# Optimization experiments

Hardware: AMD Instinct MI355X
Metric: run time of the kernel (lower is better)

Reference implementation:

```python
import jax, jax.numpy as jnp
import numpy as np
from jax import lax

# Module hyperparameters (init_kwargs)
FH, FW = 5, 5          # kernel_size
DIL_Y, DIL_X = 2, 2    # kernel_dilation
G = 2                  # num_deform_groups
F = 64                 # filters
K = FH * FW            # kernel taps


def setup_inputs() -> dict:
    key = jax.random.key(0)
    ks = jax.random.split(key, 4)
    B, H, W, C = 4, 128, 128, 32
    volume = jax.random.normal(ks[0], (B, H, W, C), jnp.float32)
    # offset-predicting conv params: offset_num = FH*FW*G*2 = 100 channels
    w_off = jax.random.normal(ks[1], (FH, FW, C, K * 2 * G), jnp.float32) * 0.01
    b_off = jnp.zeros((K * 2 * G,), jnp.float32)
    # deformable conv weights: (taps, in_channels, filters)
    w_dcn = jax.random.normal(ks[2], (K, C, F), jnp.float32) * (1.0 / np.sqrt(K * C))
    b_dcn = jnp.zeros((F,), jnp.float32)
    return {"volume": volume, "w_off": w_off, "b_off": b_off,
            "w_dcn": w_dcn, "b_dcn": b_dcn}


def _deform_conv(volume, w_off, b_off, w_dcn, b_dcn):
    B, H, W, C = volume.shape
    dp_y = DIL_Y * (FH // 2)  # dilated_pad_y
    dp_x = DIL_X * (FW // 2)  # dilated_pad_x

    # 1) dense offset conv (VALID, dilated) -> (B, oh, ow, K*2*G)
    offsets = lax.conv_general_dilated(
        volume, w_off, window_strides=(1, 1), padding='VALID',
        rhs_dilation=(DIL_Y, DIL_X),
        dimension_numbers=('NHWC', 'HWIO', 'NHWC')) + b_off
    oh, ow = offsets.shape[1], offsets.shape[2]
    off = offsets.reshape(B, oh, ow, K, 2, G)  # [..., (dy,dx), group]

    # 2) base sampling grid (stride 1): output pixel centers + dilated taps
    base_y = jnp.arange(dp_y, H - dp_y, dtype=volume.dtype)   # (oh,)
    base_x = jnp.arange(dp_x, W - dp_x, dtype=volume.dtype)   # (ow,)
    kys = jnp.arange(-dp_y, dp_y + 1, DIL_Y, dtype=volume.dtype)
    kxs = jnp.arange(-dp_x, dp_x + 1, DIL_X, dtype=volume.dtype)
    kus, kvs = jnp.meshgrid(kxs, kys)         # (FH, FW) as in source
    kdy = kvs.reshape(-1)                     # (K,)
    kdx = kus.reshape(-1)                     # (K,)

    # sample positions: (B, oh, ow, K, G)
    py = base_y[None, :, None, None, None] + kdy[None, None, None, :, None] + off[..., 0, :]
    px = base_x[None, None, :, None, None] + kdx[None, None, None, :, None] + off[..., 1, :]
    py = jnp.clip(py, 0.0, H - 1.0)
    px = jnp.clip(px, 0.0, W - 1.0)

    # 3) bilinear gather
    y0 = jnp.clip(jnp.floor(py), 0.0, H - 2.0)
    x0 = jnp.clip(jnp.floor(px), 0.0, W - 2.0)
    wy = (py - y0)[..., None]
    wx = (px - x0)[..., None]
    y0i = y0.astype(jnp.int32)
    x0i = x0.astype(jnp.int32)
    bidx = jnp.arange(B)[:, None, None, None, None]

    def gather(yy, xx):
        return volume[bidx, yy, xx]  # (B, oh, ow, K, G, C)

    v00 = gather(y0i, x0i)
    v01 = gather(y0i, x0i + 1)
    v10 = gather(y0i + 1, x0i)
    v11 = gather(y0i + 1, x0i + 1)
    sampled = (v00 * (1 - wy) * (1 - wx) + v01 * (1 - wy) * wx
               + v10 * wy * (1 - wx) + v11 * wy * wx)  # (B, oh, ow, K, G, C)

    # 4) weighted conv; deform groups partition the output filters
    wr = w_dcn.reshape(K, C, G, F // G)
    out = jnp.einsum('bhwkgc,kcgf->bhwgf', sampled, wr).reshape(B, oh, ow, F)
    return out + b_dcn


def reference(volume, w_off, b_off, w_dcn, b_dcn):
    return _deform_conv(volume, w_off, b_off, w_dcn, b_dcn)
```

## Files before the change

### kernel.cpp

```cpp
#include <hip/hip_runtime.h>
#include <hip/hip_fp16.h>

#define BB 4
#define HH 128
#define WW 128
#define CC 32
#define OH 120
#define OW 120
#define KT 25
#define OFFC 100
#define FF 64
#define NPX 32
#define NTHREADS 512

typedef __attribute__((ext_vector_type(8))) short    s16x8;
typedef __attribute__((ext_vector_type(8))) _Float16 f16x8;
typedef __attribute__((ext_vector_type(2))) _Float16 h2;
typedef __attribute__((ext_vector_type(4))) float    f32x4;

#define WB_ELEMS   (KT * 7 * 64 * 8)
#define WD_ELEMS   (4 * KT * 64 * 8)
#define VOL_UNITS  (BB * HH * WW * CC / 8)
#define VOL16_OFF  (WB_ELEMS + WD_ELEMS)

__device__ __forceinline__ short f2h(float x) {
    _Float16 h = (_Float16)x;
    return __builtin_bit_cast(short, h);
}
__device__ __forceinline__ float h2f(short x) {
    return (float)__builtin_bit_cast(_Float16, x);
}

__global__ __launch_bounds__(256) void repack_kernel(
    const float* __restrict__ volume, const float* __restrict__ w_off,
    const float* __restrict__ w_dcn, short* __restrict__ ws)
{
    int idx = blockIdx.x * 256 + threadIdx.x;
    short* WB  = ws;
    short* WD  = ws + WB_ELEMS;
    short* V16 = ws + VOL16_OFF;
    if (idx < WB_ELEMS) {
        int j = idx & 7, l = (idx >> 3) & 63;
        int tn = idx >> 9;
        int n = tn % 7, t = tn / 7;
        int c = (l >> 4) * 8 + j;
        int oc = n * 16 + (l & 15);
        float v = (oc < OFFC) ? w_off[(t * CC + c) * OFFC + oc] : 0.f;
        WB[idx] = f2h(v);
    } else if (idx < WB_ELEMS + WD_ELEMS) {
        int idx2 = idx - WB_ELEMS;
        int j = idx2 & 7, l = (idx2 >> 3) & 63;
        int nt = idx2 >> 9;
        int t = nt % KT, n = nt / KT;
        int c = (l >> 4) * 8 + j;
        int f = n * 16 + (l & 15);
        WD[idx2] = f2h(w_dcn[(t * CC + c) * FF + f]);
    } else {
        int v = idx - (WB_ELEMS + WD_ELEMS);
        if (v < VOL_UNITS) {
            const float* src = volume + (size_t)v * 8;
            float4 q0 = *(const float4*)src;
            float4 q1 = *(const float4*)(src + 4);
            alignas(16) short tmp[8];
            tmp[0] = f2h(q0.x); tmp[1] = f2h(q0.y); tmp[2] = f2h(q0.z); tmp[3] = f2h(q0.w);
            tmp[4] = f2h(q1.x); tmp[5] = f2h(q1.y); tmp[6] = f2h(q1.z); tmp[7] = f2h(q1.w);
            *(s16x8*)&V16[(size_t)v * 8] = *(const s16x8*)tmp;
        }
    }
}

__global__ __launch_bounds__(512, 2) void dcn_fused(
    const short* __restrict__ ws_ro, const float* __restrict__ b_off,
    const float* __restrict__ b_dcn, float* __restrict__ out)
{
    __shared__ __align__(16) char smem[59648];
    short* samp    = (short*)smem;
    short* patch   = (short*)smem;
    short* offtile = (short*)(smem + 53248);

    const short* WB  = ws_ro;
    const short* WD  = ws_ro + WB_ELEMS;
    const short* V16 = ws_ro + VOL16_OFF;

    const int tid  = threadIdx.x;
    const int lane = tid & 63;
    const int wv   = tid >> 6;
    const int ox0  = blockIdx.x * NPX;
    const int oy   = blockIdx.y;
    const int b    = blockIdx.z;
    const short* Vb = V16 + (size_t)b * (HH * WW * CC);

    for (int i = tid; i < 9 * 40 * 4; i += NTHREADS) {
        int cq = i & 3;
        int xi = (i >> 2) % 40;
        int yi = (i >> 2) / 40;
        int col = ox0 + xi; col = (col < WW) ? col : (WW - 1);
        s16x8 v = *(const s16x8*)&Vb[((size_t)(oy + yi) * WW + col) * CC + cq * 8];
        int u = ((yi * 40 + xi) << 2) + (cq ^ (xi & 3) ^ ((xi >> 2) & 3));
        *(s16x8*)&patch[u * 8] = v;
    }
    __syncthreads();

    if (wv < 7) {
        const int pr = lane & 15, cq = lane >> 4;
        f32x4 a0 = (f32x4){0.f, 0.f, 0.f, 0.f};
        f32x4 a1 = (f32x4){0.f, 0.f, 0.f, 0.f};
        for (int fh = 0; fh < 5; ++fh) {
            #pragma unroll
            for (int fw = 0; fw < 5; ++fw) {
                int t = fh * 5 + fw;
                int x0 = pr + 2 * fw, x1 = x0 + 16;
                f16x8 af0 = *(const f16x8*)&patch[((((2 * fh) * 40 + x0) << 2) + (cq ^ (x0 & 3) ^ ((x0 >> 2) & 3))) * 8];
                f16x8 af1 = *(const f16x8*)&patch[((((2 * fh) * 40 + x1) << 2) + (cq ^ (x1 & 3) ^ ((x1 >> 2) & 3))) * 8];
                f16x8 bf = *(const f16x8*)&WB[(t * 7 + wv) * 512 + lane * 8];
                a0 = __builtin_amdgcn_mfma_f32_16x16x32_f16(af0, bf, a0, 0, 0, 0);
                a1 = __builtin_amdgcn_mfma_f32_16x16x32_f16(af1, bf, a1, 0, 0, 0);
            }
        }
        int col = lane & 15, q = lane >> 4;
        int oc = wv * 16 + col;
        if (oc < OFFC) {
            float bo = b_off[oc];
            #pragma unroll
            for (int r = 0; r < 4; ++r) {
                offtile[(q * 4 + r) * 100 + oc]        = f2h(a0[r] + bo);
                offtile[(16 + q * 4 + r) * 100 + oc]   = f2h(a1[r] + bo);
            }
        }
    }
    __syncthreads();

    const int mt = wv & 1;
    const int ft = wv >> 1;
    const int g_ = ft >> 1;
    const int p_ = mt * 16 + (lane & 15);
    const int cq_ = lane >> 4;
    f32x4 acc = (f32x4){0.f, 0.f, 0.f, 0.f};

    for (int h = 0; h < 2; ++h) {
        const int tbase = h ? 13 : 0;
        const int ntap  = h ? 12 : 13;

        for (int u = tid; u < ntap * 256; u += NTHREADS) {
            int c  = u & 3;
            int p  = (u >> 2) & 31;
            int gg = (u >> 7) & 1;
            int tp = u >> 8;
            int t  = tbase + tp;
            int pe = (ox0 + p < OW) ? p : (OW - 1 - ox0);
            int t5 = t / 5, tm5 = t - t5 * 5;
            float dy = h2f(offtile[pe * 100 + t * 4 + gg]);
            float dx = h2f(offtile[pe * 100 + t * 4 + 2 + gg]);
            float py = (float)(oy + 2 * t5) + dy;
            float px = (float)(ox0 + pe + 2 * tm5) + dx;
            py = fminf(fmaxf(py, 0.f), 127.f);
            px = fminf(fmaxf(px, 0.f), 127.f);
            float y0f = fminf(floorf(py), 126.f);
            float x0f = fminf(floorf(px), 126.f);
            float wy = py - y0f, wx = px - x0f;
            int y0 = (int)y0f, x0i = (int)x0f;
            float w00 = (1.f - wy) * (1.f - wx);
            float w01 = (1.f - wy) * wx;
            float w10 = wy * (1.f - wx);
            float w11 = wy * wx;
            h2 W00 = (h2){(_Float16)w00, (_Float16)w00};
            h2 W01 = (h2){(_Float16)w01, (_Float16)w01};
            h2 W10 = (h2){(_Float16)w10, (_Float16)w10};
            h2 W11 = (h2){(_Float16)w11, (_Float16)w11};

            const short* vb0 = Vb + ((size_t)(y0 * WW + x0i)) * CC + c * 8;
            uint4 Au = *(const uint4*)(vb0);
            uint4 Bu = *(const uint4*)(vb0 + CC);
            uint4 Cu = *(const uint4*)(vb0 + WW * CC);
            uint4 Du = *(const uint4*)(vb0 + WW * CC + CC);

            uint4 res;
            {
                h2 r0 = __builtin_bit_cast(h2, Au.x) * W00;
                r0 = __builtin_elementwise_fma(__builtin_bit_cast(h2, Bu.x), W01, r0);
                r0 = __builtin_elementwise_fma(__builtin_bit_cast(h2, Cu.x), W10, r0);
                r0 = __builtin_elementwise_fma(__builtin_bit_cast(h2, Du.x), W11, r0);
                res.x = __builtin_bit_cast(unsigned, r0);
                h2 r1 = __builtin_bit_cast(h2, Au.y) * W00;
                r1 = __builtin_elementwise_fma(__builtin_bit_cast(h2, Bu.y), W01, r1);
                r1 = __builtin_elementwise_fma(__builtin_bit_cast(h2, Cu.y), W10, r1);
                r1 = __builtin_elementwise_fma(__builtin_bit_cast(h2, Du.y), W11, r1);
                res.y = __builtin_bit_cast(unsigned, r1);
                h2 r2 = __builtin_bit_cast(h2, Au.z) * W00;
                r2 = __builtin_elementwise_fma(__builtin_bit_cast(h2, Bu.z), W01, r2);
                r2 = __builtin_elementwise_fma(__builtin_bit_cast(h2, Cu.z), W10, r2);
                r2 = __builtin_elementwise_fma(__builtin_bit_cast(h2, Du.z), W11, r2);
                res.z = __builtin_bit_cast(unsigned, r2);
                h2 r3 = __builtin_bit_cast(h2, Au.w) * W00;
                r3 = __builtin_elementwise_fma(__builtin_bit_cast(h2, Bu.w), W01, r3);
                r3 = __builtin_elementwise_fma(__builtin_bit_cast(h2, Cu.w), W10, r3);
                r3 = __builtin_elementwise_fma(__builtin_bit_cast(h2, Du.w), W11, r3);
                res.w = __builtin_bit_cast(unsigned, r3);
            }
            int unit = (tp * 32 + p) * 8 + ((gg * 4 + c) ^ (p & 7));
            *(uint4*)&samp[unit * 8] = res;
        }
        __syncthreads();

        {
            const short* wd = WD + (ft * KT + tbase) * 512 + lane * 8;
            for (int tp = 0; tp < ntap; ++tp) {
                int unit = (tp * 32 + p_) * 8 + ((g_ * 4 + cq_) ^ (p_ & 7));
                f16x8 af = *(const f16x8*)&samp[unit * 8];
                f16x8 bf = *(const f16x8*)&wd[tp * 512];
                acc = __builtin_amdgcn_mfma_f32_16x16x32_f16(af, bf, acc, 0, 0, 0);
            }
        }
        __syncthreads();
    }

    {
        int col = lane & 15, q = lane >> 4;
        int f = ft * 16 + col;
        float bd = b_dcn[f];
        long pix0 = ((long)b * OH + oy) * OW + ox0;
        #pragma unroll
        for (int r = 0; r < 4; ++r) {
            int pp = mt * 16 + q * 4 + r;
            if (ox0 + pp < OW)
                out[(pix0 + pp) * FF + f] = acc[r] + bd;
        }
    }
}

extern "C" void kernel_launch(void* const* d_in, const int* in_sizes, int n_in,
                              void* d_out, int out_size, void* d_ws, size_t ws_size,
                              hipStream_t stream) {
    const float* volume = (const float*)d_in[0];
    const float* w_off  = (const float*)d_in[1];
    const float* b_off  = (const float*)d_in[2];
    const float* w_dcn  = (const float*)d_in[3];
    const float* b_dcn  = (const float*)d_in[4];
    float* out = (float*)d_out;
    short* ws  = (short*)d_ws;

    int repack_threads = WB_ELEMS + WD_ELEMS + VOL_UNITS;
    int repack_blocks  = (repack_threads + 255) / 256;
    repack_kernel<<<repack_blocks, 256, 0, stream>>>(volume, w_off, w_dcn, ws);

    dim3 g2((OW + NPX - 1) / NPX, OH, BB);
    dcn_fused<<<g2, NTHREADS, 0, stream>>>(ws, b_off, b_dcn, out);
}
```

Measured before the change: 127.1 us.

## Sample bilinear taps from an LDS halo window and fuse sampling into MFMA loop

Drops the fp16 copy of the whole volume made by the repack kernel. Each block now converts a 13x45 fp32 halo window straight into LDS. Bilinear taps that land inside the window are read from LDS; the rest fall back to global fp32 loads. Sample positions and weights are computed once into LDS, and each wave interpolates and feeds its result straight into two MFMAs. Tap halves are split across waves and reduced through LDS, with launch bounds raised to 4, at the cost of divergent fallback paths and higher register pressure.

Result: slower. 132.1 us (+4.0%).

```diff
diff --git a/kernel.cpp b/kernel.cpp
--- a/kernel.cpp
+++ b/kernel.cpp
@@ -13,6 +13,10 @@
 #define NPX 32
 #define NTHREADS 512
 
+#define WROWS 13
+#define WCOLS 45
+#define WUNITS (WROWS * WCOLS * 4)
+
 typedef __attribute__((ext_vector_type(8))) short    s16x8;
 typedef __attribute__((ext_vector_type(8))) _Float16 f16x8;
 typedef __attribute__((ext_vector_type(2))) _Float16 h2;
@@ -20,8 +24,6 @@
 
 #define WB_ELEMS   (KT * 7 * 64 * 8)
 #define WD_ELEMS   (4 * KT * 64 * 8)
-#define VOL_UNITS  (BB * HH * WW * CC / 8)
-#define VOL16_OFF  (WB_ELEMS + WD_ELEMS)
 
 __device__ __forceinline__ short f2h(float x) {
     _Float16 h = (_Float16)x;
@@ -30,15 +32,17 @@
 __device__ __forceinline__ float h2f(short x) {
     return (float)__builtin_bit_cast(_Float16, x);
 }
+__device__ __forceinline__ unsigned pk2(float a, float b) {
+    return ((unsigned)(unsigned short)f2h(a)) | (((unsigned)(unsigned short)f2h(b)) << 16);
+}
 
 __global__ __launch_bounds__(256) void repack_kernel(
-    const float* __restrict__ volume, const float* __restrict__ w_off,
-    const float* __restrict__ w_dcn, short* __restrict__ ws)
+    const float* __restrict__ w_off, const float* __restrict__ w_dcn,
+    short* __restrict__ ws)
 {
     int idx = blockIdx.x * 256 + threadIdx.x;
-    short* WB  = ws;
-    short* WD  = ws + WB_ELEMS;
-    short* V16 = ws + VOL16_OFF;
+    short* WB = ws;
+    short* WD = ws + WB_ELEMS;
     if (idx < WB_ELEMS) {
         int j = idx & 7, l = (idx >> 3) & 63;
         int tn = idx >> 9;
@@ -55,32 +59,26 @@
         int c = (l >> 4) * 8 + j;
         int f = n * 16 + (l & 15);
         WD[idx2] = f2h(w_dcn[(t * CC + c) * FF + f]);
-    } else {
-        int v = idx - (WB_ELEMS + WD_ELEMS);
-        if (v < VOL_UNITS) {
-            const float* src = volume + (size_t)v * 8;
-            float4 q0 = *(const float4*)src;
-            float4 q1 = *(const float4*)(src + 4);
-            alignas(16) short tmp[8];
-            tmp[0] = f2h(q0.x); tmp[1] = f2h(q0.y); tmp[2] = f2h(q0.z); tmp[3] = f2h(q0.w);
-            tmp[4] = f2h(q1.x); tmp[5] = f2h(q1.y); tmp[6] = f2h(q1.z); tmp[7] = f2h(q1.w);
-            *(s16x8*)&V16[(size_t)v * 8] = *(const s16x8*)tmp;
-        }
-    }
-}
-
-__global__ __launch_bounds__(512, 2) void dcn_fused(
-    const short* __restrict__ ws_ro, const float* __restrict__ b_off,
-    const float* __restrict__ b_dcn, float* __restrict__ out)
+    }
+}
+
+__device__ __forceinline__ int wunit(int q, int c) {
+    return q * 4 + (c ^ (q & 3));
+}
+
+__global__ __launch_bounds__(512, 4) void dcn_fused(
+    const float* __restrict__ volume, const short* __restrict__ ws_ro,
+    const float* __restrict__ b_off, const float* __restrict__ b_dcn,
+    float* __restrict__ out)
 {
-    __shared__ __align__(16) char smem[59648];
-    short* samp    = (short*)smem;
-    short* patch   = (short*)smem;
-    short* offtile = (short*)(smem + 53248);
-
-    const short* WB  = ws_ro;
-    const short* WD  = ws_ro + WB_ELEMS;
-    const short* V16 = ws_ro + VOL16_OFF;
+    __shared__ __align__(16) char smem[56640];
+    short*    window  = (short*)smem;
+    unsigned* pos4    = (unsigned*)(smem + 37440);
+    short*    offtile = (short*)(smem + 50240);
+    f32x4*    red     = (f32x4*)smem;
+
+    const short* WB = ws_ro;
+    const short* WD = ws_ro + WB_ELEMS;
 
     const int tid  = threadIdx.x;
     const int lane = tid & 63;
@@ -88,16 +86,22 @@
     const int ox0  = blockIdx.x * NPX;
     const int oy   = blockIdx.y;
     const int b    = blockIdx.z;
-    const short* Vb = V16 + (size_t)b * (HH * WW * CC);
-
-    for (int i = tid; i < 9 * 40 * 4; i += NTHREADS) {
-        int cq = i & 3;
-        int xi = (i >> 2) % 40;
-        int yi = (i >> 2) / 40;
-        int col = ox0 + xi; col = (col < WW) ? col : (WW - 1);
-        s16x8 v = *(const s16x8*)&Vb[((size_t)(oy + yi) * WW + col) * CC + cq * 8];
-        int u = ((yi * 40 + xi) << 2) + (cq ^ (xi & 3) ^ ((xi >> 2) & 3));
-        *(s16x8*)&patch[u * 8] = v;
+    const float* Vb = volume + (size_t)b * (HH * WW * CC);
+
+    for (int i = tid; i < WUNITS; i += NTHREADS) {
+        int c  = i & 3;
+        int wc = (i >> 2) % WCOLS;
+        int wr = (i >> 2) / WCOLS;
+        int gy = oy - 2 + wr;  gy = max(0, min(HH - 1, gy));
+        int gx = ox0 - 2 + wc; gx = max(0, min(WW - 1, gx));
+        const float* src = Vb + ((size_t)gy * WW + gx) * CC + c * 8;
+        float4 q0 = *(const float4*)src;
+        float4 q1 = *(const float4*)(src + 4);
+        uint4 r;
+        r.x = pk2(q0.x, q0.y); r.y = pk2(q0.z, q0.w);
+        r.z = pk2(q1.x, q1.y); r.w = pk2(q1.z, q1.w);
+        int q = wr * WCOLS + wc;
+        *(uint4*)&window[wunit(q, c) * 8] = r;
     }
     __syncthreads();
 
@@ -109,9 +113,10 @@
             #pragma unroll
             for (int fw = 0; fw < 5; ++fw) {
                 int t = fh * 5 + fw;
-                int x0 = pr + 2 * fw, x1 = x0 + 16;
-                f16x8 af0 = *(const f16x8*)&patch[((((2 * fh) * 40 + x0) << 2) + (cq ^ (x0 & 3) ^ ((x0 >> 2) & 3))) * 8];
-                f16x8 af1 = *(const f16x8*)&patch[((((2 * fh) * 40 + x1) << 2) + (cq ^ (x1 & 3) ^ ((x1 >> 2) & 3))) * 8];
+                int q0 = (2 * fh + 2) * WCOLS + (pr + 2 * fw + 2);
+                int q1 = q0 + 16;
+                f16x8 af0 = *(const f16x8*)&window[wunit(q0, cq) * 8];
+                f16x8 af1 = *(const f16x8*)&window[wunit(q1, cq) * 8];
                 f16x8 bf = *(const f16x8*)&WB[(t * 7 + wv) * 512 + lane * 8];
                 a0 = __builtin_amdgcn_mfma_f32_16x16x32_f16(af0, bf, a0, 0, 0, 0);
                 a1 = __builtin_amdgcn_mfma_f32_16x16x32_f16(af1, bf, a1, 0, 0, 0);
@@ -123,107 +128,128 @@
             float bo = b_off[oc];
             #pragma unroll
             for (int r = 0; r < 4; ++r) {
-                offtile[(q * 4 + r) * 100 + oc]        = f2h(a0[r] + bo);
-                offtile[(16 + q * 4 + r) * 100 + oc]   = f2h(a1[r] + bo);
+                offtile[(q * 4 + r) * 100 + oc]      = f2h(a0[r] + bo);
+                offtile[(16 + q * 4 + r) * 100 + oc] = f2h(a1[r] + bo);
             }
         }
     }
     __syncthreads();
 
+    for (int item = tid; item < 1600; item += NTHREADS) {
+        int p = item & 31, g = (item >> 5) & 1, t = item >> 6;
+        int pe = (ox0 + p < OW) ? p : (OW - 1 - ox0);
+        int t5 = t / 5, tm5 = t - t5 * 5;
+        float dy = h2f(offtile[pe * 100 + t * 4 + g]);
+        float dx = h2f(offtile[pe * 100 + t * 4 + 2 + g]);
+        float py = (float)(oy + 2 * t5) + dy;
+        float px = (float)(ox0 + pe + 2 * tm5) + dx;
+        py = fminf(fmaxf(py, 0.f), 127.f);
+        px = fminf(fmaxf(px, 0.f), 127.f);
+        float y0f = fminf(floorf(py), 126.f);
+        float x0f = fminf(floorf(px), 126.f);
+        float wy = py - y0f, wx = px - x0f;
+        int y0 = (int)y0f, x0i = (int)x0f;
+        int wr = y0 - oy + 2, wc = x0i - ox0 + 2;
+        unsigned inw = ((unsigned)wr <= WROWS - 2u && (unsigned)wc <= WCOLS - 2u) ? 1u : 0u;
+        int idx = ((t * 2 + g) * 32 + p) * 2;
+        pos4[idx]     = (unsigned)y0 | ((unsigned)x0i << 8) | (inw << 16);
+        pos4[idx + 1] = pk2(wy, wx);
+    }
+    __syncthreads();
+
     const int mt = wv & 1;
-    const int ft = wv >> 1;
-    const int g_ = ft >> 1;
+    const int g_ = (wv >> 1) & 1;
+    const int th = wv >> 2;
+    const int t0 = th ? 13 : 0, t1 = th ? 25 : 13;
     const int p_ = mt * 16 + (lane & 15);
-    const int cq_ = lane >> 4;
-    f32x4 acc = (f32x4){0.f, 0.f, 0.f, 0.f};
-
-    for (int h = 0; h < 2; ++h) {
-        const int tbase = h ? 13 : 0;
-        const int ntap  = h ? 12 : 13;
-
-        for (int u = tid; u < ntap * 256; u += NTHREADS) {
-            int c  = u & 3;
-            int p  = (u >> 2) & 31;
-            int gg = (u >> 7) & 1;
-            int tp = u >> 8;
-            int t  = tbase + tp;
-            int pe = (ox0 + p < OW) ? p : (OW - 1 - ox0);
-            int t5 = t / 5, tm5 = t - t5 * 5;
-            float dy = h2f(offtile[pe * 100 + t * 4 + gg]);
-            float dx = h2f(offtile[pe * 100 + t * 4 + 2 + gg]);
-            float py = (float)(oy + 2 * t5) + dy;
-            float px = (float)(ox0 + pe + 2 * tm5) + dx;
-            py = fminf(fmaxf(py, 0.f), 127.f);
-            px = fminf(fmaxf(px, 0.f), 127.f);
-            float y0f = fminf(floorf(py), 126.f);
-            float x0f = fminf(floorf(px), 126.f);
-            float wy = py - y0f, wx = px - x0f;
-            int y0 = (int)y0f, x0i = (int)x0f;
-            float w00 = (1.f - wy) * (1.f - wx);
-            float w01 = (1.f - wy) * wx;
-            float w10 = wy * (1.f - wx);
-            float w11 = wy * wx;
-            h2 W00 = (h2){(_Float16)w00, (_Float16)w00};
-            h2 W01 = (h2){(_Float16)w01, (_Float16)w01};
-            h2 W10 = (h2){(_Float16)w10, (_Float16)w10};
-            h2 W11 = (h2){(_Float16)w11, (_Float16)w11};
-
-            const short* vb0 = Vb + ((size_t)(y0 * WW + x0i)) * CC + c * 8;
-            uint4 Au = *(const uint4*)(vb0);
-            uint4 Bu = *(const uint4*)(vb0 + CC);
-            uint4 Cu = *(const uint4*)(vb0 + WW * CC);
-            uint4 Du = *(const uint4*)(vb0 + WW * CC + CC);
-
-            uint4 res;
-            {
-                h2 r0 = __builtin_bit_cast(h2, Au.x) * W00;
-                r0 = __builtin_elementwise_fma(__builtin_bit_cast(h2, Bu.x), W01, r0);
-                r0 = __builtin_elementwise_fma(__builtin_bit_cast(h2, Cu.x), W10, r0);
-                r0 = __builtin_elementwise_fma(__builtin_bit_cast(h2, Du.x), W11, r0);
-                res.x = __builtin_bit_cast(unsigned, r0);
-                h2 r1 = __builtin_bit_cast(h2, Au.y) * W00;
-                r1 = __builtin_elementwise_fma(__builtin_bit_cast(h2, Bu.y), W01, r1);
-                r1 = __builtin_elementwise_fma(__builtin_bit_cast(h2, Cu.y), W10, r1);
-                r1 = __builtin_elementwise_fma(__builtin_bit_cast(h2, Du.y), W11, r1);
-                res.y = __builtin_bit_cast(unsigned, r1);
-                h2 r2 = __builtin_bit_cast(h2, Au.z) * W00;
-                r2 = __builtin_elementwise_fma(__builtin_bit_cast(h2, Bu.z), W01, r2);
-                r2 = __builtin_elementwise_fma(__builtin_bit_cast(h2, Cu.z), W10, r2);
-                r2 = __builtin_elementwise_fma(__builtin_bit_cast(h2, Du.z), W11, r2);
-                res.z = __builtin_bit_cast(unsigned, r2);
-                h2 r3 = __builtin_bit_cast(h2, Au.w) * W00;
-                r3 = __builtin_elementwise_fma(__builtin_bit_cast(h2, Bu.w), W01, r3);
-                r3 = __builtin_elementwise_fma(__builtin_bit_cast(h2, Cu.w), W10, r3);
-                r3 = __builtin_elementwise_fma(__builtin_bit_cast(h2, Du.w), W11, r3);
-                res.w = __builtin_bit_cast(unsigned, r3);
-            }
-            int unit = (tp * 32 + p) * 8 + ((gg * 4 + c) ^ (p & 7));
-            *(uint4*)&samp[unit * 8] = res;
-        }
-        __syncthreads();
-
+    const int cq = lane >> 4;
+    const short* wd0 = WD + ((g_ * 2 + 0) * KT) * 512 + lane * 8;
+    const short* wd1 = WD + ((g_ * 2 + 1) * KT) * 512 + lane * 8;
+    f32x4 acc0 = (f32x4){0.f, 0.f, 0.f, 0.f};
+    f32x4 acc1 = (f32x4){0.f, 0.f, 0.f, 0.f};
+    const h2 oneh = (h2){(_Float16)1.f, (_Float16)1.f};
+
+    for (int t = t0; t < t1; ++t) {
+        int idx = ((t * 2 + g_) * 32 + p_) * 2;
+        unsigned pc = pos4[idx];
+        unsigned pww = pos4[idx + 1];
+        int y0 = pc & 0x7f, x0i = (pc >> 8) & 0x7f;
+
+        _Float16 wy = __builtin_bit_cast(h2, pww)[0];
+        _Float16 wx = __builtin_bit_cast(h2, pww)[1];
+        h2 vwy = (h2){wy, wy}, vwx = (h2){wx, wx};
+        h2 iwy = oneh - vwy, iwx = oneh - vwx;
+        h2 W00 = iwy * iwx, W01 = iwy * vwx, W10 = vwy * iwx, W11 = vwy * vwx;
+
+        uint4 Au, Bu, Cu, Du;
+        if (pc & 0x10000) {
+            int q00 = (y0 - oy + 2) * WCOLS + (x0i - ox0 + 2);
+            Au = *(const uint4*)&window[wunit(q00, cq) * 8];
+            Bu = *(const uint4*)&window[wunit(q00 + 1, cq) * 8];
+            Cu = *(const uint4*)&window[wunit(q00 + WCOLS, cq) * 8];
+            Du = *(const uint4*)&window[wunit(q00 + WCOLS + 1, cq) * 8];
+        } else {
+            const float* vs = Vb + ((size_t)y0 * WW + x0i) * CC + cq * 8;
+            #define LD8(dst, ptr) { float4 u0 = *(const float4*)(ptr); float4 u1 = *(const float4*)((ptr) + 4); \
+                dst.x = pk2(u0.x, u0.y); dst.y = pk2(u0.z, u0.w); dst.z = pk2(u1.x, u1.y); dst.w = pk2(u1.z, u1.w); }
+            LD8(Au, vs)
+            LD8(Bu, vs + CC)
+            LD8(Cu, vs + WW * CC)
+            LD8(Du, vs + WW * CC + CC)
+            #undef LD8
+        }
+
+        uint4 res;
         {
-            const short* wd = WD + (ft * KT + tbase) * 512 + lane * 8;
-            for (int tp = 0; tp < ntap; ++tp) {
-                int unit = (tp * 32 + p_) * 8 + ((g_ * 4 + cq_) ^ (p_ & 7));
-                f16x8 af = *(const f16x8*)&samp[unit * 8];
-                f16x8 bf = *(const f16x8*)&wd[tp * 512];
-                acc = __builtin_amdgcn_mfma_f32_16x16x32_f16(af, bf, acc, 0, 0, 0);
-            }
-        }
-        __syncthreads();
-    }
-
-    {
+            h2 r0 = __builtin_bit_cast(h2, Au.x) * W00;
+            r0 = __builtin_elementwise_fma(__builtin_bit_cast(h2, Bu.x), W01, r0);
+            r0 = __builtin_elementwise_fma(__builtin_bit_cast(h2, Cu.x), W10, r0);
+            r0 = __builtin_elementwise_fma(__builtin_bit_cast(h2, Du.x), W11, r0);
+            res.x = __builtin_bit_cast(unsigned, r0);
+            h2 r1 = __builtin_bit_cast(h2, Au.y) * W00;
+            r1 = __builtin_elementwise_fma(__builtin_bit_cast(h2, Bu.y), W01, r1);
+            r1 = __builtin_elementwise_fma(__builtin_bit_cast(h2, Cu.y), W10, r1);
+            r1 = __builtin_elementwise_fma(__builtin_bit_cast(h2, Du.y), W11, r1);
+            res.y = __builtin_bit_cast(unsigned, r1);
+            h2 r2 = __builtin_bit_cast(h2, Au.z) * W00;
+            r2 = __builtin_elementwise_fma(__builtin_bit_cast(h2, Bu.z), W01, r2);
+            r2 = __builtin_elementwise_fma(__builtin_bit_cast(h2, Cu.z), W10, r2);
+            r2 = __builtin_elementwise_fma(__builtin_bit_cast(h2, Du.z), W11, r2);
+            res.z = __builtin_bit_cast(unsigned, r2);
+            h2 r3 = __builtin_bit_cast(h2, Au.w) * W00;
+            r3 = __builtin_elementwise_fma(__builtin_bit_cast(h2, Bu.w), W01, r3);
+            r3 = __builtin_elementwise_fma(__builtin_bit_cast(h2, Cu.w), W10, r3);
+            r3 = __builtin_elementwise_fma(__builtin_bit_cast(h2, Du.w), W11, r3);
+            res.w = __builtin_bit_cast(unsigned, r3);
+        }
+        f16x8 af = __builtin_bit_cast(f16x8, res);
+        acc0 = __builtin_amdgcn_mfma_f32_16x16x32_f16(af, *(const f16x8*)&wd0[t * 512], acc0, 0, 0, 0);
+        acc1 = __builtin_amdgcn_mfma_f32_16x16x32_f16(af, *(const f16x8*)&wd1[t * 512], acc1, 0, 0, 0);
+    }
+    __syncthreads();
+
+    if (th) {
+        int slot = (mt * 2 + g_) * 2;
+        red[(slot + 0) * 64 + lane] = acc0;
+        red[(slot + 1) * 64 + lane] = acc1;
+    }
+    __syncthreads();
+    if (!th) {
+        int slot = (mt * 2 + g_) * 2;
+        acc0 += red[(slot + 0) * 64 + lane];
+        acc1 += red[(slot + 1) * 64 + lane];
         int col = lane & 15, q = lane >> 4;
-        int f = ft * 16 + col;
-        float bd = b_dcn[f];
+        int f0 = (g_ * 2 + 0) * 16 + col;
+        int f1 = (g_ * 2 + 1) * 16 + col;
+        float bd0 = b_dcn[f0], bd1 = b_dcn[f1];
         long pix0 = ((long)b * OH + oy) * OW + ox0;
         #pragma unroll
         for (int r = 0; r < 4; ++r) {
             int pp = mt * 16 + q * 4 + r;
-            if (ox0 + pp < OW)
-                out[(pix0 + pp) * FF + f] = acc[r] + bd;
+            if (ox0 + pp < OW) {
+                out[(pix0 + pp) * FF + f0] = acc0[r] + bd0;
+                out[(pix0 + pp) * FF + f1] = acc1[r] + bd1;
+            }
         }
     }
 }
@@ -239,10 +265,9 @@
     float* out = (float*)d_out;
     short* ws  = (short*)d_ws;
 
-    int repack_threads = WB_ELEMS + WD_ELEMS + VOL_UNITS;
-    int repack_blocks  = (repack_threads + 255) / 256;
-    repack_kernel<<<repack_blocks, 256, 0, stream>>>(volume, w_off, w_dcn, ws);
+    int repack_blocks = (WB_ELEMS + WD_ELEMS + 255) / 256;
+    repack_kernel<<<repack_blocks, 256, 0, stream>>>(w_off, w_dcn, ws);
 
     dim3 g2((OW + NPX - 1) / NPX, OH, BB);
-    dcn_fused<<<g2, NTHREADS, 0, stream>>>(ws, b_off, b_dcn, out);
-}
+    dcn_fused<<<g2, NTHREADS, 0, stream>>>(volume, ws, b_off, b_dcn, out);
+}
```
